# Kernel tuning notes

Hardware: AMD Instinct MI355X
Metric: run time of the kernel (lower is better)

Reference implementation:

```python
import jax, jax.numpy as jnp
import numpy as np

N = 100000
E = 1600000
IN_C = 128
HID = 128
NUM_CLASSES = 10


def setup_inputs() -> dict:
    key = jax.random.key(0)
    k1, k2, k3, k4 = jax.random.split(key, 4)
    x = jax.random.normal(k1, (N, IN_C), dtype=jnp.float32)
    edge_index = jax.random.randint(k2, (2, E), 0, N, dtype=jnp.int64)
    # PyG Linear weights are [out, in]; glorot-ish scale
    W1 = jax.random.normal(k3, (HID, IN_C), dtype=jnp.float32) / np.sqrt(IN_C)
    b1 = jnp.zeros((HID,), dtype=jnp.float32)
    W2 = jax.random.normal(k4, (NUM_CLASSES, HID), dtype=jnp.float32) / np.sqrt(HID)
    b2 = jnp.zeros((NUM_CLASSES,), dtype=jnp.float32)
    return {"x": x, "edge_index": edge_index, "W1": W1, "b1": b1, "W2": W2, "b2": b2}


def _gcn_conv(x, W, b, row, col, n):
    """Faithful PyG GCNConv: linear transform, symmetric gcn_norm with self-loops,
    gather-scale-scatter aggregation, then bias."""
    h = x @ W.T  # [N, out]
    # add self loops
    loop = jnp.arange(n, dtype=row.dtype)
    r = jnp.concatenate([row, loop])
    c = jnp.concatenate([col, loop])
    # degree at destination (col), edge weight = 1
    deg = jax.ops.segment_sum(jnp.ones(r.shape[0], dtype=h.dtype), c, num_segments=n)
    dis = jnp.where(deg > 0, jax.lax.rsqrt(deg), 0.0)
    norm = dis[r] * dis[c]  # [E+N]
    msgs = norm[:, None] * h[r]  # gather + scale, [E+N, out]
    out = jax.ops.segment_sum(msgs, c, num_segments=n)  # scatter-add
    return out + b


def reference(x, edge_index, W1, b1, W2, b2):
    row, col = edge_index[0], edge_index[1]
    n = x.shape[0]
    x = _gcn_conv(x, W1, b1, row, col, n)
    x = _gcn_conv(x, W2, b2, row, col, n)
    return x
```

## Files before the change

kernel.cpp:

```cpp
#include <hip/hip_runtime.h>
#include <hip/hip_fp16.h>

#define N_NODES 100000
#define E_EDGES 1600000
#define NCLS 10

#define BW 256
#define NB 391
#define EPB 8192
#define NBLK_BIN 196
#define BUCK_CAP 6144

__global__ __launch_bounds__(256) void k_hist_w12(const int* __restrict__ col,
                                                  int* __restrict__ blockHist,
                                                  const float* __restrict__ W1,
                                                  const float* __restrict__ W2,
                                                  const float* __restrict__ b1,
                                                  float* __restrict__ W12,
                                                  float* __restrict__ c1) {
    __shared__ int   h[NB];
    __shared__ float w2s[1280];
    int t = threadIdx.x;
    if (blockIdx.x < NBLK_BIN) {
        for (int i = t; i < NB; i += 256) h[i] = 0;
        __syncthreads();
        int base = blockIdx.x * EPB;
        int end  = min(base + EPB, E_EDGES);
        for (int e = base + t; e < end; e += 256)
            atomicAdd(&h[col[e] >> 8], 1);
        __syncthreads();
        for (int i = t; i < NB; i += 256)
            blockHist[blockIdx.x * NB + i] = h[i];
    } else {
        for (int i = t; i < 1280; i += 256) w2s[i] = W2[i];
        __syncthreads();
        if (t < 128) {
            float acc[NCLS];
            #pragma unroll
            for (int j = 0; j < NCLS; ++j) acc[j] = 0.f;
            for (int m = 0; m < 128; ++m) {
                float w1mk = W1[m * 128 + t];
                #pragma unroll
                for (int j = 0; j < NCLS; ++j) acc[j] += w2s[j * 128 + m] * w1mk;
            }
            #pragma unroll
            for (int j = 0; j < NCLS; ++j) W12[j * 128 + t] = acc[j];
        } else if (t < 144) {
            int j = t - 128;
            float acc = 0.f;
            if (j < NCLS)
                for (int m = 0; m < 128; ++m) acc += W2[j * 128 + m] * b1[m];
            c1[j] = (j < NCLS) ? acc : 0.f;
        }
    }
}

__global__ __launch_bounds__(256) void k_colscan(int* __restrict__ blockHist,
                                                 int* __restrict__ bucketTotal) {
    __shared__ int s[256];
    int i = blockIdx.x;
    int t = threadIdx.x;
    int v = (t < NBLK_BIN) ? blockHist[t * NB + i] : 0;
    s[t] = v;
    __syncthreads();
    for (int st = 1; st < 256; st <<= 1) {
        int tmp = (t >= st) ? s[t - st] : 0;
        __syncthreads();
        s[t] += tmp;
        __syncthreads();
    }
    if (t < NBLK_BIN) blockHist[t * NB + i] = s[t] - v;
    if (t == 255) bucketTotal[i] = s[255];
}

__global__ __launch_bounds__(512) void k_bin_g1(const int* __restrict__ ei,
                                                const int* __restrict__ blockHist,
                                                const int* __restrict__ bucketTotal,
                                                unsigned* __restrict__ binned,
                                                const float* __restrict__ x,
                                                const float* __restrict__ W12,
                                                float* __restrict__ g1u) {
    __shared__ int h[NB];
    __shared__ int lofs[NB];
    __shared__ int chunk[NB];
    __shared__ int s[512];
    __shared__ unsigned staged[EPB];
    int t = threadIdx.x;
    if (blockIdx.x < NBLK_BIN) {
        if (t < NB) h[t] = 0;
        __syncthreads();
        int base = blockIdx.x * EPB;
        int end  = min(base + EPB, E_EDGES);
        const int* col = ei + E_EDGES;
        for (int e = base + t; e < end; e += 512)
            atomicAdd(&h[col[e] >> 8], 1);
        __syncthreads();
        int hv = (t < NB) ? h[t] : 0;
        s[t] = hv;
        __syncthreads();
        for (int st = 1; st < 512; st <<= 1) {
            int tmp = (t >= st) ? s[t - st] : 0;
            __syncthreads();
            s[t] += tmp;
            __syncthreads();
        }
        if (t < NB) lofs[t] = s[t] - hv;
        __syncthreads();
        int bv = (t < NB) ? bucketTotal[t] : 0;
        s[t] = bv;
        __syncthreads();
        for (int st = 1; st < 512; st <<= 1) {
            int tmp = (t >= st) ? s[t - st] : 0;
            __syncthreads();
            s[t] += tmp;
            __syncthreads();
        }
        if (t < NB) {
            chunk[t] = (s[t] - bv) + blockHist[blockIdx.x * NB + t];
            h[t] = 0;
        }
        __syncthreads();
        for (int e = base + t; e < end; e += 512) {
            int c = col[e];
            int r = ei[e];
            int b = c >> 8;
            int rank = atomicAdd(&h[b], 1);
            staged[lofs[b] + rank] = ((unsigned)r << 8) | (unsigned)(c & 255);
        }
        __syncthreads();
        int wid  = t >> 6;
        int lane = t & 63;
        for (int b = wid; b < NB; b += 8) {
            int lo  = lofs[b];
            int len = h[b];
            int gb  = chunk[b];
            for (int i = lane; i < len; i += 64)
                binned[gb + i] = staged[lo + i];
        }
    } else {
        int row = (blockIdx.x - NBLK_BIN) * 512 + t;
        if (row >= N_NODES) return;

        const float4* x4 = (const float4*)x;
        float acc[NCLS];
        #pragma unroll
        for (int j = 0; j < NCLS; ++j) acc[j] = 0.f;

        #pragma unroll
        for (int k4 = 0; k4 < 32; ++k4) {
            float4 xv = x4[row * 32 + k4];
            #pragma unroll
            for (int j = 0; j < NCLS; ++j) {
                const float* wj = &W12[j * 128 + k4 * 4];
                acc[j] += xv.x * wj[0] + xv.y * wj[1] + xv.z * wj[2] + xv.w * wj[3];
            }
        }

        float4* dst = (float4*)&g1u[row * 16];
        dst[0] = make_float4(acc[0], acc[1], acc[2], acc[3]);
        dst[1] = make_float4(acc[4], acc[5], acc[6], acc[7]);
        dst[2] = make_float4(acc[8], acc[9], 0.f, 0.f);
    }
}

__global__ __launch_bounds__(256) void k_build(const unsigned* __restrict__ binned,
                                               const int* __restrict__ bucketTotal,
                                               int2* __restrict__ od,
                                               float* __restrict__ dis,
                                               int* __restrict__ csr,
                                               const float* __restrict__ g1u,
                                               __half2* __restrict__ g1h) {
    __shared__ int red[256];
    __shared__ int cnt[BW];
    __shared__ int sc[BW];
    __shared__ int eoff[BW];
    __shared__ int cur[BW];
    __shared__ int stg[BUCK_CAP];
    int k = blockIdx.x;
    int t = threadIdx.x;

    int part = 0;
    for (int i = t; i < k; i += 256) part += bucketTotal[i];
    red[t] = part;
    cnt[t] = 0;
    __syncthreads();
    for (int st = 128; st; st >>= 1) {
        if (t < st) red[t] += red[t + st];
        __syncthreads();
    }
    int s0 = red[0];
    int s1 = s0 + bucketTotal[k];

    for (int i = s0 + t; i < s1; i += 256)
        atomicAdd(&cnt[binned[i] & 255], 1);
    __syncthreads();
    int v = cnt[t];
    sc[t] = v;
    __syncthreads();
    for (int st = 1; st < 256; st <<= 1) {
        int tmp = (t >= st) ? sc[t - st] : 0;
        __syncthreads();
        sc[t] += tmp;
        __syncthreads();
    }
    eoff[t] = sc[t] - v;
    cur[t] = 0;
    int node = k * BW + t;
    float d = rsqrtf((float)(v + 1));
    if (node < N_NODES) {
        od[node] = make_int2(s0 + eoff[t], v);
        dis[node] = d;

        const float4* g4 = (const float4*)&g1u[node * 16];
        float4 a = g4[0];
        float4 b = g4[1];
        float4 c = g4[2];
        __half2 hp[8];
        hp[0] = __floats2half2_rn(d * a.x, d * a.y);
        hp[1] = __floats2half2_rn(d * a.z, d * a.w);
        hp[2] = __floats2half2_rn(d * b.x, d * b.y);
        hp[3] = __floats2half2_rn(d * b.z, d * b.w);
        hp[4] = __floats2half2_rn(d * c.x, d * c.y);
        hp[5] = __floats2half2_rn(0.f, 0.f);
        hp[6] = hp[5];
        hp[7] = hp[5];
        uint4* dst = (uint4*)&g1h[node * 8];
        dst[0] = *(const uint4*)&hp[0];
        dst[1] = *(const uint4*)&hp[4];
    }
    __syncthreads();
    for (int i = s0 + t; i < s1; i += 256) {
        unsigned p = binned[i];
        int lc = p & 255;
        int r  = p >> 8;
        int pos = eoff[lc] + atomicAdd(&cur[lc], 1);
        stg[pos] = r;
    }
    __syncthreads();
    int len = s1 - s0;
    for (int i = t; i < len; i += 256)
        csr[s0 + i] = stg[i];
}

__global__ __launch_bounds__(256) void k_agg_a(const __half2* __restrict__ g1h,
                                               const float* __restrict__ dis,
                                               const int* __restrict__ csr,
                                               const int2* __restrict__ od,
                                               const float* __restrict__ c1,
                                               __half2* __restrict__ h2h) {
    int c = blockIdx.x * 32 + (threadIdx.x >> 3);
    int j = threadIdx.x & 7;
    if (c >= N_NODES) return;

    float2 acc = __half22float2(g1h[c * 8 + j]);

    int2 odv  = od[c];
    int start = odv.x;
    int deg   = odv.y;
    int k = 0;
    if (deg >= 4) {
        int i0 = csr[start + 0], i1 = csr[start + 1];
        int i2 = csr[start + 2], i3 = csr[start + 3];
        for (; k + 8 <= deg; k += 4) {
            int n0 = csr[start + k + 4], n1 = csr[start + k + 5];
            int n2 = csr[start + k + 6], n3 = csr[start + k + 7];
            float2 a0 = __half22float2(g1h[i0 * 8 + j]);
            float2 a1 = __half22float2(g1h[i1 * 8 + j]);
            float2 a2 = __half22float2(g1h[i2 * 8 + j]);
            float2 a3 = __half22float2(g1h[i3 * 8 + j]);
            acc.x += (a0.x + a1.x) + (a2.x + a3.x);
            acc.y += (a0.y + a1.y) + (a2.y + a3.y);
            i0 = n0; i1 = n1; i2 = n2; i3 = n3;
        }
        float2 a0 = __half22float2(g1h[i0 * 8 + j]);
        float2 a1 = __half22float2(g1h[i1 * 8 + j]);
        float2 a2 = __half22float2(g1h[i2 * 8 + j]);
        float2 a3 = __half22float2(g1h[i3 * 8 + j]);
        acc.x += (a0.x + a1.x) + (a2.x + a3.x);
        acc.y += (a0.y + a1.y) + (a2.y + a3.y);
        k += 4;
    }
    for (; k < deg; ++k) {
        float2 a = __half22float2(g1h[csr[start + k] * 8 + j]);
        acc.x += a.x;
        acc.y += a.y;
    }

    float dc = dis[c];
    float ox = dc * (dc * acc.x + c1[2 * j]);
    float oy = dc * (dc * acc.y + c1[2 * j + 1]);
    h2h[c * 8 + j] = __floats2half2_rn(ox, oy);
}

__global__ __launch_bounds__(256) void k_agg_b(const __half2* __restrict__ h2h,
                                               const float* __restrict__ dis,
                                               const int* __restrict__ csr,
                                               const int2* __restrict__ od,
                                               const float* __restrict__ b2,
                                               float* __restrict__ out) {
    int c = blockIdx.x * 32 + (threadIdx.x >> 3);
    int j = threadIdx.x & 7;
    if (c >= N_NODES) return;

    float2 acc = __half22float2(h2h[c * 8 + j]);

    int2 odv  = od[c];
    int start = odv.x;
    int deg   = odv.y;
    int k = 0;
    if (deg >= 4) {
        int i0 = csr[start + 0], i1 = csr[start + 1];
        int i2 = csr[start + 2], i3 = csr[start + 3];
        for (; k + 8 <= deg; k += 4) {
            int n0 = csr[start + k + 4], n1 = csr[start + k + 5];
            int n2 = csr[start + k + 6], n3 = csr[start + k + 7];
            float2 a0 = __half22float2(h2h[i0 * 8 + j]);
            float2 a1 = __half22float2(h2h[i1 * 8 + j]);
            float2 a2 = __half22float2(h2h[i2 * 8 + j]);
            float2 a3 = __half22float2(h2h[i3 * 8 + j]);
            acc.x += (a0.x + a1.x) + (a2.x + a3.x);
            acc.y += (a0.y + a1.y) + (a2.y + a3.y);
            i0 = n0; i1 = n1; i2 = n2; i3 = n3;
        }
        float2 a0 = __half22float2(h2h[i0 * 8 + j]);
        float2 a1 = __half22float2(h2h[i1 * 8 + j]);
        float2 a2 = __half22float2(h2h[i2 * 8 + j]);
        float2 a3 = __half22float2(h2h[i3 * 8 + j]);
        acc.x += (a0.x + a1.x) + (a2.x + a3.x);
        acc.y += (a0.y + a1.y) + (a2.y + a3.y);
        k += 4;
    }
    for (; k < deg; ++k) {
        float2 a = __half22float2(h2h[csr[start + k] * 8 + j]);
        acc.x += a.x;
        acc.y += a.y;
    }

    if (j < 5) {
        float dc = dis[c];
        float2 o;
        o.x = dc * acc.x + b2[2 * j];
        o.y = dc * acc.y + b2[2 * j + 1];
        *(float2*)&out[c * NCLS + 2 * j] = o;
    }
}

extern "C" void kernel_launch(void* const* d_in, const int* in_sizes, int n_in,
                              void* d_out, int out_size, void* d_ws, size_t ws_size,
                              hipStream_t stream) {
    const float* x  = (const float*)d_in[0];
    const int*   ei = (const int*)d_in[1];
    const float* W1 = (const float*)d_in[2];
    const float* b1 = (const float*)d_in[3];
    const float* W2 = (const float*)d_in[4];
    const float* b2 = (const float*)d_in[5];
    float* out = (float*)d_out;

    char* ws = (char*)d_ws;
    int*      bucketTotal = (int*)(ws + 8192);
    float*    W12         = (float*)(ws + 16384);
    float*    c1          = (float*)(ws + 24576);
    int*      blockHist   = (int*)(ws + 32768);
    int2*     od          = (int2*)(ws + (1 << 20));
    float*    dis         = (float*)(ws + (3 << 20));
    unsigned* binned      = (unsigned*)(ws + (4 << 20));
    int*      csr         = (int*)(ws + (12 << 20));
    float*    g1u         = (float*)(ws + (20 << 20));
    __half2*  g1h         = (__half2*)(ws + (28 << 20));
    __half2*  h2h         = (__half2*)(ws + (32 << 20));

    k_hist_w12<<<NBLK_BIN + 1, 256, 0, stream>>>(ei + E_EDGES, blockHist,
                                                 W1, W2, b1, W12, c1);
    k_colscan<<<NB, 256, 0, stream>>>(blockHist, bucketTotal);
    k_bin_g1<<<NBLK_BIN + 196, 512, 0, stream>>>(ei, blockHist, bucketTotal,
                                                 binned, x, W12, g1u);
    k_build<<<NB, 256, 0, stream>>>(binned, bucketTotal, od, dis, csr, g1u, g1h);

    k_agg_a<<<(N_NODES + 31) / 32, 256, 0, stream>>>(g1h, dis, csr, od, c1, h2h);
    k_agg_b<<<(N_NODES + 31) / 32, 256, 0, stream>>>(h2h, dis, csr, od, b2, out);
}
```

Baseline: 93.30 us.

## Widen binning kernel to 1024 threads, merge scans, flatten scatter write-out

```diff
diff --git a/kernel.cpp b/kernel.cpp
--- a/kernel.cpp
+++ b/kernel.cpp
@@ -73,18 +73,19 @@
     if (t == 255) bucketTotal[i] = s[255];
 }
 
-__global__ __launch_bounds__(512) void k_bin_g1(const int* __restrict__ ei,
-                                                const int* __restrict__ blockHist,
-                                                const int* __restrict__ bucketTotal,
-                                                unsigned* __restrict__ binned,
-                                                const float* __restrict__ x,
-                                                const float* __restrict__ W12,
-                                                float* __restrict__ g1u) {
+__global__ __launch_bounds__(1024) void k_bin_g1(const int* __restrict__ ei,
+                                                 const int* __restrict__ blockHist,
+                                                 const int* __restrict__ bucketTotal,
+                                                 unsigned* __restrict__ binned,
+                                                 const float* __restrict__ x,
+                                                 const float* __restrict__ W12,
+                                                 float* __restrict__ g1u) {
     __shared__ int h[NB];
     __shared__ int lofs[NB];
     __shared__ int chunk[NB];
-    __shared__ int s[512];
+    __shared__ int s[1024];
     __shared__ unsigned staged[EPB];
+    __shared__ int slotL[EPB];
     int t = threadIdx.x;
     if (blockIdx.x < NBLK_BIN) {
         if (t < NB) h[t] = 0;
@@ -92,53 +93,44 @@
         int base = blockIdx.x * EPB;
         int end  = min(base + EPB, E_EDGES);
         const int* col = ei + E_EDGES;
-        for (int e = base + t; e < end; e += 512)
+        for (int e = base + t; e < end; e += 1024)
             atomicAdd(&h[col[e] >> 8], 1);
         __syncthreads();
-        int hv = (t < NB) ? h[t] : 0;
-        s[t] = hv;
-        __syncthreads();
-        for (int st = 1; st < 512; st <<= 1) {
-            int tmp = (t >= st) ? s[t - st] : 0;
+        int u = t & 511;
+        int v;
+        if (t < 512) v = (u < NB) ? h[u] : 0;
+        else         v = (u < NB) ? bucketTotal[u] : 0;
+        s[t] = v;
+        __syncthreads();
+        for (int st = 1; st <= 256; st <<= 1) {
+            int tmp = (u >= st) ? s[t - st] : 0;
             __syncthreads();
             s[t] += tmp;
             __syncthreads();
         }
-        if (t < NB) lofs[t] = s[t] - hv;
-        __syncthreads();
-        int bv = (t < NB) ? bucketTotal[t] : 0;
-        s[t] = bv;
-        __syncthreads();
-        for (int st = 1; st < 512; st <<= 1) {
-            int tmp = (t >= st) ? s[t - st] : 0;
-            __syncthreads();
-            s[t] += tmp;
-            __syncthreads();
-        }
-        if (t < NB) {
-            chunk[t] = (s[t] - bv) + blockHist[blockIdx.x * NB + t];
-            h[t] = 0;
-        }
-        __syncthreads();
-        for (int e = base + t; e < end; e += 512) {
+        if (t < 512) {
+            if (u < NB) lofs[u] = s[t] - v;
+        } else if (u < NB) {
+            chunk[u] = (s[t] - v) + blockHist[blockIdx.x * NB + u];
+        }
+        __syncthreads();
+        if (t < NB) h[t] = 0;
+        __syncthreads();
+        for (int e = base + t; e < end; e += 1024) {
             int c = col[e];
             int r = ei[e];
             int b = c >> 8;
             int rank = atomicAdd(&h[b], 1);
-            staged[lofs[b] + rank] = ((unsigned)r << 8) | (unsigned)(c & 255);
-        }
-        __syncthreads();
-        int wid  = t >> 6;
-        int lane = t & 63;
-        for (int b = wid; b < NB; b += 8) {
-            int lo  = lofs[b];
-            int len = h[b];
-            int gb  = chunk[b];
-            for (int i = lane; i < len; i += 64)
-                binned[gb + i] = staged[lo + i];
-        }
+            int lpos = lofs[b] + rank;
+            staged[lpos] = ((unsigned)r << 8) | (unsigned)(c & 255);
+            slotL[lpos] = chunk[b] + rank;
+        }
+        __syncthreads();
+        int ne = end - base;
+        for (int i = t; i < ne; i += 1024)
+            binned[slotL[i]] = staged[i];
     } else {
-        int row = (blockIdx.x - NBLK_BIN) * 512 + t;
+        int row = (blockIdx.x - NBLK_BIN) * 1024 + t;
         if (row >= N_NODES) return;
 
         const float4* x4 = (const float4*)x;
@@ -372,7 +364,7 @@
     k_hist_w12<<<NBLK_BIN + 1, 256, 0, stream>>>(ei + E_EDGES, blockHist,
                                                  W1, W2, b1, W12, c1);
     k_colscan<<<NB, 256, 0, stream>>>(blockHist, bucketTotal);
-    k_bin_g1<<<NBLK_BIN + 196, 512, 0, stream>>>(ei, blockHist, bucketTotal,
+    k_bin_g1<<<NBLK_BIN + 98, 1024, 0, stream>>>(ei, blockHist, bucketTotal,
                                                  binned, x, W12, g1u);
     k_build<<<NB, 256, 0, stream>>>(binned, bucketTotal, od, dis, csr, g1u, g1h);
 
```

Measured after the change: 105.4 us. +13.0%, slower.
